# Optimization experiments

Measured on AMD Instinct MI355X. Metric: run time of the kernel, lower is better.

## Reference

```python
import jax, jax.numpy as jnp
import numpy as np

NEG_INF = -9e15


def setup_inputs() -> dict:
    key = jax.random.key(0)
    k1, k2, k3, k4, k5, k6 = jax.random.split(key, 6)
    B, N, F_IN, F_OUT = 16, 2048, 256, 128
    inputs = jax.random.normal(k1, (B, N, F_IN), dtype=jnp.float32)
    adj_matrix = jax.random.randint(k2, (B, N, N), 0, 2, dtype=jnp.int32)
    W = jax.random.normal(k3, (F_OUT, F_IN), dtype=jnp.float32) * (1.0 / np.sqrt(F_IN))
    b_W = jax.random.normal(k4, (F_OUT,), dtype=jnp.float32) * 0.02
    a = jax.random.normal(k5, (1, 2 * F_OUT), dtype=jnp.float32) * (1.0 / np.sqrt(2 * F_OUT))
    b_a = jax.random.normal(k6, (1,), dtype=jnp.float32) * 0.02
    return {"inputs": inputs, "adj_matrix": adj_matrix, "W": W, "b_W": b_W, "a": a, "b_a": b_a}


def reference(inputs, adj_matrix, W, b_W, a, b_a):
    # wh: [B, N, H]
    wh = jnp.einsum('bnf,hf->bnh', inputs, W) + b_W
    H = wh.shape[-1]
    # linear_self_W([wh_i, wh_j]) = a1.wh_i + a2.wh_j + b  (rank-1 linear over concat)
    a1 = a[0, :H]
    a2 = a[0, H:]
    src = jnp.einsum('bnh,h->bn', wh, a1)  # [B, N] contribution of row node i
    dst = jnp.einsum('bnh,h->bn', wh, a2)  # [B, N] contribution of col node j
    e = jax.nn.leaky_relu(src[:, :, None] + dst[:, None, :] + b_a[0], negative_slope=0.01)
    e = jnp.where(adj_matrix > 0, e, NEG_INF)
    att = jax.nn.softmax(e, axis=-1)  # dropout in eval mode = identity
    return jax.nn.elu(jnp.einsum('bij,bjh->bih', att, wh))
```

## Files before the change

kernel.cpp:

```cpp
#include <hip/hip_runtime.h>
#include <hip/hip_bf16.h>


#define BDIM 16
#define NDIM 2048
#define FIN 256
#define HDIM 128
#define LOG2E 1.4426950408889634f

typedef short short8 __attribute__((ext_vector_type(8)));
typedef float floatx4 __attribute__((ext_vector_type(4)));
typedef int intx4 __attribute__((ext_vector_type(4)));

__device__ __forceinline__ unsigned short f2bf(float x) {
    unsigned int u = __float_as_uint(x);
    unsigned int r = (u + 0x7fffu + ((u >> 16) & 1u)) >> 16;
    return (unsigned short)r;
}
__device__ __forceinline__ float bf2f(unsigned short s) {
    return __uint_as_float(((unsigned int)s) << 16);
}
__device__ __forceinline__ intx4 ldnt(const int* p) {
    return __builtin_nontemporal_load(reinterpret_cast<const intx4*>(p));
}

__global__ __launch_bounds__(256) void k_wh(const float* __restrict__ X,
                                            const float* __restrict__ W,
                                            const float* __restrict__ bW,
                                            const float* __restrict__ a,
                                            const float* __restrict__ ba_p,
                                            float* __restrict__ src,
                                            float* __restrict__ dst,
                                            unsigned short* __restrict__ whF) {
    __shared__ short lds[27648];
    short (*ah)[72] = (short(*)[72])lds;
    short (*al)[72] = (short(*)[72])(lds + 4608);
    short (*bh)[72] = (short(*)[72])(lds + 9216);
    short (*bl)[72] = (short(*)[72])(lds + 18432);
    short (*tb)[72] = (short(*)[72])lds;

    const int tid = threadIdx.x;
    const long row0 = (long)blockIdx.x * 64;
    const int w = tid >> 6, lane = tid & 63;
    const int lm = lane & 15, q = lane >> 4;
    const float ba0 = ba_p[0];

    float a1v[8], a2v[8], bwv[8];
    #pragma unroll
    for (int nt = 0; nt < 8; nt++) {
        a1v[nt] = a[nt * 16 + lm];
        a2v[nt] = a[HDIM + nt * 16 + lm];
        bwv[nt] = bW[nt * 16 + lm];
    }

    floatx4 acc[8];
    #pragma unroll
    for (int nt = 0; nt < 8; nt++) acc[nt] = (floatx4){0.f, 0.f, 0.f, 0.f};

    for (int k0 = 0; k0 < FIN; k0 += 64) {
        #pragma unroll
        for (int u = 0; u < 4; u++) {
            int idx = tid + u * 256;
            int r = idx >> 4, fc = (idx & 15) * 4;
            float4 v = *reinterpret_cast<const float4*>(X + (row0 + r) * FIN + k0 + fc);
            union { unsigned short s[4]; uint2 u2; } ph, pl;
            ph.s[0] = f2bf(v.x); pl.s[0] = f2bf(v.x - bf2f(ph.s[0]));
            ph.s[1] = f2bf(v.y); pl.s[1] = f2bf(v.y - bf2f(ph.s[1]));
            ph.s[2] = f2bf(v.z); pl.s[2] = f2bf(v.z - bf2f(ph.s[2]));
            ph.s[3] = f2bf(v.w); pl.s[3] = f2bf(v.w - bf2f(ph.s[3]));
            *reinterpret_cast<uint2*>(&ah[r][fc]) = ph.u2;
            *reinterpret_cast<uint2*>(&al[r][fc]) = pl.u2;
        }
        #pragma unroll
        for (int u = 0; u < 8; u++) {
            int idx = tid + u * 256;
            int hh = idx >> 4, fc = (idx & 15) * 4;
            float4 v = *reinterpret_cast<const float4*>(W + hh * FIN + k0 + fc);
            union { unsigned short s[4]; uint2 u2; } ph, pl;
            ph.s[0] = f2bf(v.x); pl.s[0] = f2bf(v.x - bf2f(ph.s[0]));
            ph.s[1] = f2bf(v.y); pl.s[1] = f2bf(v.y - bf2f(ph.s[1]));
            ph.s[2] = f2bf(v.z); pl.s[2] = f2bf(v.z - bf2f(ph.s[2]));
            ph.s[3] = f2bf(v.w); pl.s[3] = f2bf(v.w - bf2f(ph.s[3]));
            *reinterpret_cast<uint2*>(&bh[hh][fc]) = ph.u2;
            *reinterpret_cast<uint2*>(&bl[hh][fc]) = pl.u2;
        }
        __syncthreads();
        #pragma unroll
        for (int ks = 0; ks < 64; ks += 32) {
            short8 afh = *reinterpret_cast<const short8*>(&ah[w * 16 + lm][ks + q * 8]);
            short8 afl = *reinterpret_cast<const short8*>(&al[w * 16 + lm][ks + q * 8]);
            #pragma unroll
            for (int nt = 0; nt < 8; nt++) {
                short8 bfh = *reinterpret_cast<const short8*>(&bh[nt * 16 + lm][ks + q * 8]);
                short8 bfl = *reinterpret_cast<const short8*>(&bl[nt * 16 + lm][ks + q * 8]);
                acc[nt] = __builtin_amdgcn_mfma_f32_16x16x32_bf16(afh, bfh, acc[nt], 0, 0, 0);
                acc[nt] = __builtin_amdgcn_mfma_f32_16x16x32_bf16(afh, bfl, acc[nt], 0, 0, 0);
                acc[nt] = __builtin_amdgcn_mfma_f32_16x16x32_bf16(afl, bfh, acc[nt], 0, 0, 0);
            }
        }
        __syncthreads();
    }

    float s1[4] = {0.f, 0.f, 0.f, 0.f}, s2[4] = {0.f, 0.f, 0.f, 0.f};
    #pragma unroll
    for (int nt = 0; nt < 8; nt++) {
        #pragma unroll
        for (int r = 0; r < 4; r++) {
            float v = acc[nt][r] + bwv[nt];
            s1[r] += v * a1v[nt];
            s2[r] += v * a2v[nt];
            tb[nt * 16 + lm][w * 16 + q * 4 + r] = f2bf(v);
        }
    }
    #pragma unroll
    for (int r = 0; r < 4; r++) {
        #pragma unroll
        for (int o = 1; o < 16; o <<= 1) {
            s1[r] += __shfl_xor(s1[r], o);
            s2[r] += __shfl_xor(s2[r], o);
        }
    }
    if (lm == 0) {
        #pragma unroll
        for (int r = 0; r < 4; r++) {
            long row = row0 + w * 16 + q * 4 + r;
            src[row] = (s1[r] + ba0) * LOG2E;
            dst[row] = s2[r] * LOG2E;
        }
    }
    __syncthreads();
    const int b = (int)(row0 >> 11);
    const int jc0 = (int)((row0 & 2047) >> 5);
    const int f = tid >> 4;
    const int sub = tid & 15;
    const int jcrel = f >> 3, ht = f & 7;
    const size_t fbase = (((size_t)b * 64 + jc0 + jcrel) * 8 + ht) * 512;
    #pragma unroll
    for (int i = 0; i < 4; i++) {
        int l = sub * 4 + i;
        uint4 v = *reinterpret_cast<const uint4*>(&tb[ht * 16 + (l & 15)][jcrel * 32 + (l >> 4) * 8]);
        *reinterpret_cast<uint4*>(whF + fbase + l * 8) = v;
    }
}


#define BAR()                                                                  \
    do {                                                                       \
        asm volatile("s_waitcnt lgkmcnt(0)" ::: "memory");                     \
        __builtin_amdgcn_s_barrier();                                          \
    } while (0)

#define ADJ_ISSUE(GNEXT, H)                                                    \
    do {                                                                       \
        _Pragma("unroll")                                                      \
        for (int r = 0; r < 8; r++) {                                          \
            const int* ap = adj +                                              \
                (size_t)(rowbase + wave * 16 + (H) * 8 + r) * NDIM +           \
                (GNEXT) * 256 + lane * 4;                                      \
            av[r] = ldnt(ap);                                                  \
        }                                                                      \
    } while (0)

#define ADJ_BALLOT(GNEXT, H)                                                   \
    do {                                                                       \
        _Pragma("unroll")                                                      \
        for (int r = 0; r < 8; r++) {                                          \
            unsigned long long b0 = __ballot(av[r][0] != 0);                   \
            unsigned long long b1 = __ballot(av[r][1] != 0);                   \
            unsigned long long b2 = __ballot(av[r][2] != 0);                   \
            unsigned long long b3 = __ballot(av[r][3] != 0);                   \
            if (lane < 8) {                                                    \
                unsigned long long bb = (lane < 2) ? b0                        \
                                        : (lane < 4) ? b1                      \
                                        : (lane < 6) ? b2 : b3;                \
                unsigned wv = (lane & 1) ? (unsigned)(bb >> 32) : (unsigned)bb;\
                maskB[(GNEXT) & 1][lane][wave * 16 + (H) * 8 + r] = wv;        \
            }                                                                  \
        }                                                                      \
    } while (0)

#define COMP(T, BUF, C)                                                        \
    do {                                                                       \
        const int hi = ((C) & 4) ? 1 : 0;                                      \
        const int GB = (g8 >> 3) & 1;                                          \
        unsigned m0 = maskB[GB][0 + hi][wrow];                                 \
        unsigned m1 = maskB[GB][2 + hi][wrow];                                 \
        unsigned m2 = maskB[GB][4 + hi][wrow];                                 \
        unsigned m3 = maskB[GB][6 + hi][wrow];                                 \
        floatx4 dd0 = *reinterpret_cast<const floatx4*>(&dstS[(T) * 32 + q8]); \
        floatx4 dd1 =                                                          \
            *reinterpret_cast<const floatx4*>(&dstS[(T) * 32 + q8 + 4]);       \
        const int base = 8 * ((C) & 3) + 2 * q;                                \
        short8 af;                                                             \
        _Pragma("unroll")                                                      \
        for (int j = 0; j < 8; j++) {                                          \
            float x = si + ((j >> 2) ? dd1[j & 3] : dd0[j & 3]);               \
            x = fmaxf(x, 0.01f * x);               \
            float e2 = __builtin_amdgcn_exp2f(x);                              \
            unsigned mw = (j & 3) == 0 ? m0 : (j & 3) == 1 ? m1                \
                           : (j & 3) == 2 ? m2 : m3;                           \
            unsigned bit = (mw >> (base + (j >> 2))) & 1u;                     \
            float wgt = bit ? e2 : 0.f;                                        \
            lpart += wgt;                                                      \
            __hip_bfloat16 hb = __float2bfloat16(wgt);        \
            af[j] = *reinterpret_cast<short*>(&hb);                            \
        }                                                                      \
        _Pragma("unroll")                                                      \
        for (int hj = 0; hj < 8; hj++) {                                       \
            short8 fb = *reinterpret_cast<const short8*>(                      \
                &whS[BUF][hj * 512 + lane * 8]);                               \
            acc[hj] = __builtin_amdgcn_mfma_f32_16x16x32_bf16(af, fb,          \
                                                              acc[hj], 0, 0, 0); \
        }                                                                      \
    } while (0)

#define PAIR(PI)                                                               \
    do {                                                                       \
        const int T = g8 + (PI) * 2;                                           \
        constexpr int BUF0 = ((PI) & 1) * 2;                                   \
        constexpr int WBUF = ((((PI) & 1)) ^ 1) * 2;                           \
        short8 s0, s1, s2, s3;                                                 \
        if (T + 2 < 64) {       \
            const unsigned short* gp = gsrc + (size_t)(T + 2) * 4096;          \
            s0 = *reinterpret_cast<const short8*>(gp);                         \
            s1 = *reinterpret_cast<const short8*>(gp + 512);                   \
            s2 = *reinterpret_cast<const short8*>(gp + 4096);                  \
            s3 = *reinterpret_cast<const short8*>(gp + 4096 + 512);            \
        }                                                                      \
        if ((PI) == 0 && g8 < 56) ADJ_ISSUE((g8 >> 3) + 1, 0);                 \
        if ((PI) == 1 && g8 < 56) {                                            \
            ADJ_BALLOT((g8 >> 3) + 1, 0);                                      \
            ADJ_ISSUE((g8 >> 3) + 1, 1);                                       \
        }                                                                      \
        if ((PI) == 3 && g8 < 56) ADJ_BALLOT((g8 >> 3) + 1, 1);                \
        COMP(T, BUF0, (PI) * 2);                                               \
        COMP(T + 1, BUF0 + 1, (PI) * 2 + 1);                                   \
        if (T + 2 < 64) {    \
            *reinterpret_cast<short8*>(&whS[WBUF][pofs]) = s0;                 \
            *reinterpret_cast<short8*>(&whS[WBUF][pofs + 512]) = s1;           \
            *reinterpret_cast<short8*>(&whS[WBUF + 1][pofs]) = s2;             \
            *reinterpret_cast<short8*>(&whS[WBUF + 1][pofs + 512]) = s3;       \
        }                                                                      \
        BAR();                                                                 \
    } while (0)

__global__ __launch_bounds__(256) void k_attn(const int* __restrict__ adj,
                                              const unsigned short* __restrict__ whF,
                                              const float* __restrict__ src,
                                              const float* __restrict__ dst,
                                              float* __restrict__ out) {
    __shared__ short whS[4][4096];
    __shared__ unsigned maskB[2][8][65];
    __shared__ float dstS[2048];
    __shared__ float lred[64];
    __shared__ float linv_s[64];

    const int tid = threadIdx.x;
    const int bid = ((int)blockIdx.x & 7) * 64 + ((int)blockIdx.x >> 3);
    const int b = bid >> 5;
    const int i0 = (bid & 31) * 64;
    const int wave = tid >> 6, lane = tid & 63;
    const int lm = lane & 15, q = lane >> 4;
    const int q8 = q * 8;
    const int wrow = wave * 16 + lm;
    const int rowbase = b * NDIM + i0;

    const float si = src[rowbase + wrow];
    const unsigned short* gsrc =
        whF + (size_t)b * 262144 + wave * 1024 + lane * 8;
    const int pofs = wave * 1024 + lane * 8;

    floatx4 acc[8];
    #pragma unroll
    for (int hj = 0; hj < 8; hj++) acc[hj] = (floatx4){0.f, 0.f, 0.f, 0.f};
    float lpart = 0.f;

    intx4 av[8];

    {
        const float* dg = dst + b * NDIM;
        *reinterpret_cast<float4*>(&dstS[tid * 8]) =
            *reinterpret_cast<const float4*>(dg + tid * 8);
        *reinterpret_cast<float4*>(&dstS[tid * 8 + 4]) =
            *reinterpret_cast<const float4*>(dg + tid * 8 + 4);
    }
    {
        short8 p0 = *reinterpret_cast<const short8*>(gsrc);
        short8 p1 = *reinterpret_cast<const short8*>(gsrc + 512);
        short8 p2 = *reinterpret_cast<const short8*>(gsrc + 4096);
        short8 p3 = *reinterpret_cast<const short8*>(gsrc + 4096 + 512);
        *reinterpret_cast<short8*>(&whS[0][pofs]) = p0;
        *reinterpret_cast<short8*>(&whS[0][pofs + 512]) = p1;
        *reinterpret_cast<short8*>(&whS[1][pofs]) = p2;
        *reinterpret_cast<short8*>(&whS[1][pofs + 512]) = p3;
    }
    ADJ_ISSUE(0, 0);
    ADJ_BALLOT(0, 0);
    ADJ_ISSUE(0, 1);
    ADJ_BALLOT(0, 1);
    __syncthreads();

    for (int g8 = 0; g8 < 64; g8 += 8) {
        PAIR(0); PAIR(1); PAIR(2); PAIR(3);
    }

    lpart += __shfl_xor(lpart, 16);
    lpart += __shfl_xor(lpart, 32);
    if (q == 0) lred[wrow] = lpart;
    __syncthreads();
    if (tid < 64) {
        float l = lred[tid];
        linv_s[tid] = l > 0.f ? 1.f / l : 0.f;
    }
    __syncthreads();

    #pragma unroll
    for (int r = 0; r < 4; r++) {
        int il = wave * 16 + q * 4 + r;
        float li = linv_s[il];
        size_t obase = ((size_t)(rowbase + il)) * HDIM + lm;
        #pragma unroll
        for (int hj = 0; hj < 8; hj++) {
            float x = acc[hj][r] * li;
            x = x > 0.f ? x : (__expf(x) - 1.f);
            out[obase + hj * 16] = x;
        }
    }
}

extern "C" void kernel_launch(void* const* d_in, const int* in_sizes, int n_in,
                              void* d_out, int out_size, void* d_ws, size_t ws_size,
                              hipStream_t stream) {
    const float* X  = (const float*)d_in[0];
    const int* adj  = (const int*)d_in[1];
    const float* W  = (const float*)d_in[2];
    const float* bW = (const float*)d_in[3];
    const float* a  = (const float*)d_in[4];
    const float* ba = (const float*)d_in[5];
    float* out = (float*)d_out;

    float* srcv = (float*)d_ws;
    float* dstv = srcv + BDIM * NDIM;
    unsigned short* whF = (unsigned short*)(dstv + BDIM * NDIM);

    k_wh<<<BDIM * NDIM / 64, 256, 0, stream>>>(X, W, bW, a, ba, srcv, dstv, whF);
    k_attn<<<BDIM * (NDIM / 64), 256, 0, stream>>>(adj, whF, srcv, dstv, out);
}
```

Baseline: 397.7 us.

## Process four tiles per barrier with deeper LDS double-buffering and MFMA priority

Restructures the attention main loop from pairs of tiles to quads, doubling the wh LDS staging buffer to 8 slots so each barrier covers four tiles and global prefetch runs four tiles ahead. The adjacency ballot/issue schedule is reshuffled to fit the two-step loop. It also raises wave priority around the MFMA block with s_setprio. This halves barrier count and increases prefetch depth, at the cost of more LDS (lower occupancy possible) and more registers for the staged loads.

Measured after the change: 396.5 us. Within noise of the previous version (-0.3%).

```diff
diff --git a/kernel.cpp b/kernel.cpp
--- a/kernel.cpp
+++ b/kernel.cpp
@@ -205,6 +205,7 @@
             __hip_bfloat16 hb = __float2bfloat16(wgt);        \
             af[j] = *reinterpret_cast<short*>(&hb);                            \
         }                                                                      \
+        __builtin_amdgcn_s_setprio(1);             \
         _Pragma("unroll")                                                      \
         for (int hj = 0; hj < 8; hj++) {                                       \
             short8 fb = *reinterpret_cast<const short8*>(                      \
@@ -212,34 +213,48 @@
             acc[hj] = __builtin_amdgcn_mfma_f32_16x16x32_bf16(af, fb,          \
                                                               acc[hj], 0, 0, 0); \
         }                                                                      \
-    } while (0)
-
-#define PAIR(PI)                                                               \
-    do {                                                                       \
-        const int T = g8 + (PI) * 2;                                           \
-        constexpr int BUF0 = ((PI) & 1) * 2;                                   \
-        constexpr int WBUF = ((((PI) & 1)) ^ 1) * 2;                           \
-        short8 s0, s1, s2, s3;                                                 \
-        if (T + 2 < 64) {       \
-            const unsigned short* gp = gsrc + (size_t)(T + 2) * 4096;          \
+        __builtin_amdgcn_s_setprio(0);                                         \
+    } while (0)
+
+#define QUAD(QI)                                                               \
+    do {                                                                       \
+        const int T0 = g8 + (QI) * 4;                                          \
+        constexpr int RBUF = (QI) * 4;                                         \
+        constexpr int WBUF = 4 - (QI) * 4;                                     \
+        short8 s0, s1, s2, s3, s4, s5, s6, s7;                                 \
+        if (T0 + 4 < 64) {          \
+            const unsigned short* gp = gsrc + (size_t)(T0 + 4) * 4096;         \
             s0 = *reinterpret_cast<const short8*>(gp);                         \
             s1 = *reinterpret_cast<const short8*>(gp + 512);                   \
             s2 = *reinterpret_cast<const short8*>(gp + 4096);                  \
             s3 = *reinterpret_cast<const short8*>(gp + 4096 + 512);            \
-        }                                                                      \
-        if ((PI) == 0 && g8 < 56) ADJ_ISSUE((g8 >> 3) + 1, 0);                 \
-        if ((PI) == 1 && g8 < 56) {                                            \
-            ADJ_BALLOT((g8 >> 3) + 1, 0);                                      \
-            ADJ_ISSUE((g8 >> 3) + 1, 1);                                       \
-        }                                                                      \
-        if ((PI) == 3 && g8 < 56) ADJ_BALLOT((g8 >> 3) + 1, 1);                \
-        COMP(T, BUF0, (PI) * 2);                                               \
-        COMP(T + 1, BUF0 + 1, (PI) * 2 + 1);                                   \
-        if (T + 2 < 64) {    \
+            s4 = *reinterpret_cast<const short8*>(gp + 8192);                  \
+            s5 = *reinterpret_cast<const short8*>(gp + 8192 + 512);            \
+            s6 = *reinterpret_cast<const short8*>(gp + 12288);                 \
+            s7 = *reinterpret_cast<const short8*>(gp + 12288 + 512);           \
+        }                                                                      \
+        if ((QI) == 0) {                                                       \
+            if (g8 > 0) ADJ_BALLOT(g8 >> 3, 1);       \
+            if (g8 < 56) ADJ_ISSUE((g8 >> 3) + 1, 0);                          \
+        } else {                                                               \
+            if (g8 < 56) {                                                     \
+                ADJ_BALLOT((g8 >> 3) + 1, 0);                                  \
+                ADJ_ISSUE((g8 >> 3) + 1, 1);                                   \
+            }                                                                  \
+        }                                                                      \
+        COMP(T0, RBUF + 0, (QI) * 4 + 0);                                      \
+        COMP(T0 + 1, RBUF + 1, (QI) * 4 + 1);                                  \
+        COMP(T0 + 2, RBUF + 2, (QI) * 4 + 2);                                  \
+        COMP(T0 + 3, RBUF + 3, (QI) * 4 + 3);                                  \
+        if (T0 + 4 < 64) {  \
             *reinterpret_cast<short8*>(&whS[WBUF][pofs]) = s0;                 \
             *reinterpret_cast<short8*>(&whS[WBUF][pofs + 512]) = s1;           \
             *reinterpret_cast<short8*>(&whS[WBUF + 1][pofs]) = s2;             \
             *reinterpret_cast<short8*>(&whS[WBUF + 1][pofs + 512]) = s3;       \
+            *reinterpret_cast<short8*>(&whS[WBUF + 2][pofs]) = s4;             \
+            *reinterpret_cast<short8*>(&whS[WBUF + 2][pofs + 512]) = s5;       \
+            *reinterpret_cast<short8*>(&whS[WBUF + 3][pofs]) = s6;             \
+            *reinterpret_cast<short8*>(&whS[WBUF + 3][pofs + 512]) = s7;       \
         }                                                                      \
         BAR();                                                                 \
     } while (0)
@@ -249,7 +264,7 @@
                                               const float* __restrict__ src,
                                               const float* __restrict__ dst,
                                               float* __restrict__ out) {
-    __shared__ short whS[4][4096];
+    __shared__ short whS[8][4096];
     __shared__ unsigned maskB[2][8][65];
     __shared__ float dstS[2048];
     __shared__ float lred[64];
@@ -289,10 +304,18 @@
         short8 p1 = *reinterpret_cast<const short8*>(gsrc + 512);
         short8 p2 = *reinterpret_cast<const short8*>(gsrc + 4096);
         short8 p3 = *reinterpret_cast<const short8*>(gsrc + 4096 + 512);
+        short8 p4 = *reinterpret_cast<const short8*>(gsrc + 8192);
+        short8 p5 = *reinterpret_cast<const short8*>(gsrc + 8192 + 512);
+        short8 p6 = *reinterpret_cast<const short8*>(gsrc + 12288);
+        short8 p7 = *reinterpret_cast<const short8*>(gsrc + 12288 + 512);
         *reinterpret_cast<short8*>(&whS[0][pofs]) = p0;
         *reinterpret_cast<short8*>(&whS[0][pofs + 512]) = p1;
         *reinterpret_cast<short8*>(&whS[1][pofs]) = p2;
         *reinterpret_cast<short8*>(&whS[1][pofs + 512]) = p3;
+        *reinterpret_cast<short8*>(&whS[2][pofs]) = p4;
+        *reinterpret_cast<short8*>(&whS[2][pofs + 512]) = p5;
+        *reinterpret_cast<short8*>(&whS[3][pofs]) = p6;
+        *reinterpret_cast<short8*>(&whS[3][pofs + 512]) = p7;
     }
     ADJ_ISSUE(0, 0);
     ADJ_BALLOT(0, 0);
@@ -301,7 +324,8 @@
     __syncthreads();
 
     for (int g8 = 0; g8 < 64; g8 += 8) {
-        PAIR(0); PAIR(1); PAIR(2); PAIR(3);
+        QUAD(0);
+        QUAD(1);
     }
 
     lpart += __shfl_xor(lpart, 16);
```
